# Performance work log

Hardware: AMD Instinct MI355X
Metric: run time of the kernel (lower is better)

## Reference

```python
import jax, jax.numpy as jnp
import numpy as np

EPS = 1e-8  # torch CosineSimilarity default eps


def setup_inputs() -> dict:
    key = jax.random.key(0)
    ks = jax.random.split(key, 9)
    B, C, H, W = 8, 256, 96, 96
    co = C // 2
    s = 0.05
    return {
        "x": jax.random.normal(ks[0], (B, C, H, W), dtype=jnp.float32),
        "w_theta": jax.random.normal(ks[1], (co, C), dtype=jnp.float32) * s,
        "b_theta": jax.random.normal(ks[2], (co,), dtype=jnp.float32) * s,
        "w_phi": jax.random.normal(ks[3], (co, C), dtype=jnp.float32) * s,
        "b_phi": jax.random.normal(ks[4], (co,), dtype=jnp.float32) * s,
        "w_g": jax.random.normal(ks[5], (co, C), dtype=jnp.float32) * s,
        "b_g": jax.random.normal(ks[6], (co,), dtype=jnp.float32) * s,
        "w_back": jax.random.normal(ks[7], (C, co), dtype=jnp.float32) * s,
        "b_back": jax.random.normal(ks[8], (C,), dtype=jnp.float32) * s,
    }


def reference(x, w_theta, b_theta, w_phi, b_phi, w_g, b_g, w_back, b_back):
    B, C, H, W = x.shape
    # replicate pad, then gather the 9 (3x3) shifted views: [B, C, 9, H, W]
    xp = jnp.pad(x, ((0, 0), (0, 0), (1, 1), (1, 1)), mode="edge")
    neigh = jnp.stack(
        [xp[:, :, i:i + H, j:j + W] for i in range(3) for j in range(3)], axis=2
    )
    # 1x1 convs are per-pixel linear maps
    theta = jnp.einsum("bchw,oc->bohw", x, w_theta) + b_theta[None, :, None, None]
    phi = jnp.einsum("bcnhw,oc->bonhw", neigh, w_phi) + b_phi[None, :, None, None, None]
    g = jnp.einsum("bcnhw,oc->bonhw", neigh, w_g) + b_g[None, :, None, None, None]
    # cosine similarity over channel dim o: [B, 9, H, W]
    dot = jnp.sum(phi * theta[:, :, None], axis=1)
    denom = jnp.maximum(
        jnp.sqrt(jnp.sum(phi * phi, axis=1)) * jnp.sqrt(jnp.sum(theta * theta, axis=1))[:, None],
        EPS,
    )
    attn = jax.nn.softmax(dot / denom, axis=1)  # softmax over 9 neighbors
    # weighted average of g over neighbors: [B, co, H, W]
    wa = jnp.einsum("bonhw,bnhw->bohw", g, attn)
    x_res = jnp.einsum("bohw,co->bchw", wa, w_back) + b_back[None, :, None, None]
    return x + x_res
```

## Files before the change

### kernel.cpp

```cpp
#include <hip/hip_runtime.h>
#include <hip/hip_bf16.h>
#include <math.h>

#define HW   9216
#define WIMG 96
#define NPIX 73728
#define CIN  256
#define CO   128

typedef __attribute__((ext_vector_type(8))) short short8v;
typedef __attribute__((ext_vector_type(8))) unsigned short u16x8;
typedef __attribute__((ext_vector_type(4))) float f32x4;

__device__ __forceinline__ unsigned short f2bf(float f) {
    __hip_bfloat16 h = __float2bfloat16(f);
    return __builtin_bit_cast(unsigned short, h);
}
__device__ __forceinline__ float bf2f(unsigned short u) {
    unsigned v = ((unsigned)u) << 16;
    return __builtin_bit_cast(float, v);
}

__device__ __forceinline__ int swz(int row, int kk2 ) {
    return (row * 128 + kk2) ^ ((row & 7) << 4);
}

__global__ __launch_bounds__(256) void k1_mfma(
    const float* __restrict__ x,
    const float* __restrict__ wt, const float* __restrict__ bt,
    const float* __restrict__ wp, const float* __restrict__ bp,
    const float* __restrict__ wg, const float* __restrict__ bg,
    unsigned short* __restrict__ th, unsigned short* __restrict__ ph,
    unsigned short* __restrict__ gf)
{
    __shared__ char As[128 * 128];
    __shared__ char Bs[128 * 128];

    const int t   = threadIdx.x;
    const int bid = blockIdx.x;
    const int lb  = (bid & 7) * 216 + (bid >> 3);
    const int nb  = lb % 3;
    const int bx  = lb / 3;

    const float* W  = (nb == 0) ? wt : (nb == 1) ? wp : wg;
    const float* Bv = (nb == 0) ? bt : (nb == 1) ? bp : bg;
    unsigned short* O = (nb == 0) ? th : (nb == 1) ? ph : gf;

    const int P0 = bx * 128;
    const int b  = P0 / HW;
    const int p0 = P0 - b * HW;
    const float* xb = x + (size_t)b * CIN * HW + p0;

    const int wid = t >> 6, lane = t & 63;
    const int wm = (wid & 1) * 64, wn = (wid >> 1) * 64;
    const int l15 = lane & 15, lg = lane >> 4;

    f32x4 acc[4][4] = {};

    for (int kt = 0; kt < CIN; kt += 64) {
        if (kt) __syncthreads();
        #pragma unroll
        for (int it = 0; it < 8; ++it) {
            int kq = ((t >> 4) & 3) + (it & 3) * 4;
            int pp = (t & 15) + ((t >> 6) << 4) + ((it >> 2) << 6);
            ushort4 v;
            v.x = f2bf(xb[(size_t)(kt + kq * 4 + 0) * HW + pp]);
            v.y = f2bf(xb[(size_t)(kt + kq * 4 + 1) * HW + pp]);
            v.z = f2bf(xb[(size_t)(kt + kq * 4 + 2) * HW + pp]);
            v.w = f2bf(xb[(size_t)(kt + kq * 4 + 3) * HW + pp]);
            *(ushort4*)(As + swz(pp, kq * 8)) = v;
        }
        #pragma unroll
        for (int it = 0; it < 8; ++it) {
            int kq = t & 15;
            int n  = (t >> 4) + it * 16;
            float4 w4 = *(const float4*)(W + (size_t)n * CIN + kt + kq * 4);
            ushort4 v;
            v.x = f2bf(w4.x); v.y = f2bf(w4.y); v.z = f2bf(w4.z); v.w = f2bf(w4.w);
            *(ushort4*)(Bs + swz(n, kq * 8)) = v;
        }
        __syncthreads();
        #pragma unroll
        for (int ks = 0; ks < 2; ++ks) {
            const int kk2 = ks * 64 + lg * 16;
            short8v a[4], bq[4];
            #pragma unroll
            for (int mt = 0; mt < 4; ++mt)
                a[mt] = *(const short8v*)(As + swz(wm + mt * 16 + l15, kk2));
            #pragma unroll
            for (int nt = 0; nt < 4; ++nt)
                bq[nt] = *(const short8v*)(Bs + swz(wn + nt * 16 + l15, kk2));
            #pragma unroll
            for (int mt = 0; mt < 4; ++mt)
                #pragma unroll
                for (int nt = 0; nt < 4; ++nt)
                    acc[mt][nt] = __builtin_amdgcn_mfma_f32_16x16x32_bf16(
                        a[mt], bq[nt], acc[mt][nt], 0, 0, 0);
        }
    }

    float bias[4];
    #pragma unroll
    for (int nt = 0; nt < 4; ++nt) bias[nt] = Bv[wn + nt * 16 + l15];
    #pragma unroll
    for (int mt = 0; mt < 4; ++mt)
        #pragma unroll
        for (int j = 0; j < 4; ++j) {
            size_t row = (size_t)(P0 + wm + mt * 16 + lg * 4 + j) * CO;
            #pragma unroll
            for (int nt = 0; nt < 4; ++nt)
                O[row + wn + nt * 16 + l15] = f2bf(acc[mt][nt][j] + bias[nt]);
        }
}

__global__ __launch_bounds__(256) void k_attn(
    const unsigned short* __restrict__ th, const unsigned short* __restrict__ ph,
    const unsigned short* __restrict__ gf, unsigned short* __restrict__ wa)
{
    const int t   = threadIdx.x;
    const int bid = blockIdx.x;
    const int lb  = (bid & 7) * 144 + (bid >> 3);
    const int s = t >> 2, q = t & 3;
    const int P = lb * 64 + s;
    const int b = P / HW;
    const int p = P - b * HW;
    const int h = p / WIMG;
    const int w = p - h * WIMG;
    const size_t ib = (size_t)b * HW;

    const u16x8* tv = (const u16x8*)(th + (size_t)P * CO + q * 32);
    float T32[32];
    #pragma unroll
    for (int j = 0; j < 4; ++j) {
        u16x8 v = tv[j];
        #pragma unroll
        for (int e = 0; e < 8; ++e) T32[j * 8 + e] = bf2f(v[e]);
    }
    float tt = 0.f;
    #pragma unroll
    for (int k = 0; k < 32; ++k) tt = fmaf(T32[k], T32[k], tt);
    tt += __shfl_xor(tt, 1);
    tt += __shfl_xor(tt, 2);
    const float st = sqrtf(tt);

    float score[9];
    #pragma unroll
    for (int n = 0; n < 9; ++n) {
        int hh = h + n / 3 - 1; hh = hh < 0 ? 0 : (hh > 95 ? 95 : hh);
        int w2 = w + n % 3 - 1; w2 = w2 < 0 ? 0 : (w2 > 95 ? 95 : w2);
        const u16x8* pv = (const u16x8*)(ph + (ib + hh * WIMG + w2) * CO + q * 32);
        float d = 0.f, pp = 0.f;
        #pragma unroll
        for (int j = 0; j < 4; ++j) {
            u16x8 v = pv[j];
            #pragma unroll
            for (int e = 0; e < 8; ++e) {
                float f = bf2f(v[e]);
                d  = fmaf(T32[j * 8 + e], f, d);
                pp = fmaf(f, f, pp);
            }
        }
        d  += __shfl_xor(d, 1);  d  += __shfl_xor(d, 2);
        pp += __shfl_xor(pp, 1); pp += __shfl_xor(pp, 2);
        float den = fmaxf(sqrtf(pp) * st, 1e-8f);
        score[n] = d / den;
    }

    float mx = score[0];
    #pragma unroll
    for (int n = 1; n < 9; ++n) mx = fmaxf(mx, score[n]);
    float sum = 0.f;
    #pragma unroll
    for (int n = 0; n < 9; ++n) { score[n] = expf(score[n] - mx); sum += score[n]; }
    const float inv = 1.f / sum;

    float acc[32];
    #pragma unroll
    for (int k = 0; k < 32; ++k) acc[k] = 0.f;

    #pragma unroll
    for (int n = 0; n < 9; ++n) {
        int hh = h + n / 3 - 1; hh = hh < 0 ? 0 : (hh > 95 ? 95 : hh);
        int w2 = w + n % 3 - 1; w2 = w2 < 0 ? 0 : (w2 > 95 ? 95 : w2);
        const u16x8* gv = (const u16x8*)(gf + (ib + hh * WIMG + w2) * CO + q * 32);
        float a = score[n] * inv;
        #pragma unroll
        for (int j = 0; j < 4; ++j) {
            u16x8 v = gv[j];
            #pragma unroll
            for (int e = 0; e < 8; ++e)
                acc[j * 8 + e] = fmaf(a, bf2f(v[e]), acc[j * 8 + e]);
        }
    }

    u16x8* ov = (u16x8*)(wa + (size_t)P * CO + q * 32);
    #pragma unroll
    for (int j = 0; j < 4; ++j) {
        u16x8 o;
        #pragma unroll
        for (int e = 0; e < 8; ++e) o[e] = f2bf(acc[j * 8 + e]);
        ov[j] = o;
    }
}

__global__ __launch_bounds__(256) void k3_mfma(
    const unsigned short* __restrict__ wa, const float* __restrict__ wb,
    const float* __restrict__ bb_, const float* __restrict__ x,
    float* __restrict__ out)
{
    __shared__ char As[128 * 128];
    __shared__ char Bs[128 * 128];

    const int t   = threadIdx.x;
    const int bid = blockIdx.x;
    const int lb  = (bid & 7) * 144 + (bid >> 3);
    const int cb  = (lb & 1) * 128;
    const int P0  = (lb >> 1) * 128;
    const int b   = P0 / HW;
    const int p0  = P0 - b * HW;

    const int wid = t >> 6, lane = t & 63;
    const int wm = (wid & 1) * 64, wn = (wid >> 1) * 64;
    const int l15 = lane & 15, lg = lane >> 4;

    f32x4 acc[4][4] = {};

    for (int kt = 0; kt < CO; kt += 64) {
        if (kt) __syncthreads();
        #pragma unroll
        for (int it = 0; it < 8; ++it) {
            int kq = t & 15;
            int n  = (t >> 4) + it * 16;
            float4 w4 = *(const float4*)(wb + (size_t)(cb + n) * CO + kt + kq * 4);
            ushort4 v;
            v.x = f2bf(w4.x); v.y = f2bf(w4.y); v.z = f2bf(w4.z); v.w = f2bf(w4.w);
            *(ushort4*)(As + swz(n, kq * 4 * 2)) = v;
        }
        #pragma unroll
        for (int it = 0; it < 4; ++it) {
            int kq = t & 7;
            int n  = (t >> 3) + it * 32;
            u16x8 u = *(const u16x8*)(wa + (size_t)(P0 + n) * CO + kt + kq * 8);
            *(u16x8*)(Bs + swz(n, kq * 16)) = u;
        }
        __syncthreads();
        #pragma unroll
        for (int ks = 0; ks < 2; ++ks) {
            const int kk2 = ks * 64 + lg * 16;
            short8v a[4], bq[4];
            #pragma unroll
            for (int mt = 0; mt < 4; ++mt)
                a[mt] = *(const short8v*)(As + swz(wm + mt * 16 + l15, kk2));
            #pragma unroll
            for (int nt = 0; nt < 4; ++nt)
                bq[nt] = *(const short8v*)(Bs + swz(wn + nt * 16 + l15, kk2));
            #pragma unroll
            for (int mt = 0; mt < 4; ++mt)
                #pragma unroll
                for (int nt = 0; nt < 4; ++nt)
                    acc[mt][nt] = __builtin_amdgcn_mfma_f32_16x16x32_bf16(
                        a[mt], bq[nt], acc[mt][nt], 0, 0, 0);
        }
    }

    #pragma unroll
    for (int mt = 0; mt < 4; ++mt)
        #pragma unroll
        for (int j = 0; j < 4; ++j) {
            int ch = cb + wm + mt * 16 + lg * 4 + j;
            size_t base = ((size_t)b * CIN + ch) * HW + p0;
            float bias = bb_[ch];
            #pragma unroll
            for (int nt = 0; nt < 4; ++nt) {
                int px = wn + nt * 16 + l15;
                out[base + px] = x[base + px] + acc[mt][nt][j] + bias;
            }
        }
}

extern "C" void kernel_launch(void* const* d_in, const int* in_sizes, int n_in,
                              void* d_out, int out_size, void* d_ws, size_t ws_size,
                              hipStream_t stream)
{
    const float* x  = (const float*)d_in[0];
    const float* wt = (const float*)d_in[1];
    const float* bt = (const float*)d_in[2];
    const float* wp = (const float*)d_in[3];
    const float* bp = (const float*)d_in[4];
    const float* wg = (const float*)d_in[5];
    const float* bg = (const float*)d_in[6];
    const float* wb = (const float*)d_in[7];
    const float* bb = (const float*)d_in[8];
    float* out = (float*)d_out;

    const size_t FEAT = (size_t)NPIX * CO;
    unsigned short* th = (unsigned short*)d_ws;
    unsigned short* ph = th + FEAT;
    unsigned short* gf = ph + FEAT;
    unsigned short* wa = gf + FEAT;

    hipLaunchKernelGGL(k1_mfma, dim3(1728), dim3(256), 0, stream,
                       x, wt, bt, wp, bp, wg, bg, th, ph, gf);
    hipLaunchKernelGGL(k_attn, dim3(1152), dim3(256), 0, stream,
                       th, ph, gf, wa);
    hipLaunchKernelGGL(k3_mfma, dim3(1152), dim3(256), 0, stream,
                       wa, wb, bb, x, out);
}
```

Before: 234.4 us.

## Load x tile once per block and reuse it across theta/phi/g projections

The first GEMM kernel now stages the full 128-pixel by 256-channel x tile in LDS as bf16 (64KB) and loops over the three projection weight sets inside one block. Previously each projection launched its own block that re-read and re-converted x. The grid shrinks from 1728 to 576 blocks, which cuts global x traffic threefold but raises LDS use and lowers occupancy and parallelism. The attention kernel also precomputes neighbor offsets, splits the dot-product reductions into four partial accumulators, and uses the fast __expf.

Result: slower. 256.3 us (+9.3%).

```diff
diff --git a/kernel.cpp b/kernel.cpp
--- a/kernel.cpp
+++ b/kernel.cpp
@@ -21,8 +21,11 @@
     return __builtin_bit_cast(float, v);
 }
 
-__device__ __forceinline__ int swz(int row, int kk2 ) {
-    return (row * 128 + kk2) ^ ((row & 7) << 4);
+__device__ __forceinline__ int swz(int row, int kb) {
+    return (row * 128) + (kb ^ ((row & 7) << 4));
+}
+__device__ __forceinline__ int swzA(int row, int kb) {
+    return (row * 512) + (kb ^ ((row & 7) << 4));
 }
 
 __global__ __launch_bounds__(256) void k1_mfma(
@@ -33,32 +36,22 @@
     unsigned short* __restrict__ th, unsigned short* __restrict__ ph,
     unsigned short* __restrict__ gf)
 {
-    __shared__ char As[128 * 128];
+    __shared__ char As[128 * 512];
     __shared__ char Bs[128 * 128];
 
     const int t   = threadIdx.x;
     const int bid = blockIdx.x;
-    const int lb  = (bid & 7) * 216 + (bid >> 3);
-    const int nb  = lb % 3;
-    const int bx  = lb / 3;
-
-    const float* W  = (nb == 0) ? wt : (nb == 1) ? wp : wg;
-    const float* Bv = (nb == 0) ? bt : (nb == 1) ? bp : bg;
-    unsigned short* O = (nb == 0) ? th : (nb == 1) ? ph : gf;
-
-    const int P0 = bx * 128;
-    const int b  = P0 / HW;
-    const int p0 = P0 - b * HW;
+    const int lb  = (bid & 7) * 72 + (bid >> 3);
+    const int P0  = lb * 128;
+    const int b   = P0 / HW;
+    const int p0  = P0 - b * HW;
     const float* xb = x + (size_t)b * CIN * HW + p0;
 
     const int wid = t >> 6, lane = t & 63;
     const int wm = (wid & 1) * 64, wn = (wid >> 1) * 64;
     const int l15 = lane & 15, lg = lane >> 4;
 
-    f32x4 acc[4][4] = {};
-
     for (int kt = 0; kt < CIN; kt += 64) {
-        if (kt) __syncthreads();
         #pragma unroll
         for (int it = 0; it < 8; ++it) {
             int kq = ((t >> 4) & 3) + (it & 3) * 4;
@@ -68,49 +61,62 @@
             v.y = f2bf(xb[(size_t)(kt + kq * 4 + 1) * HW + pp]);
             v.z = f2bf(xb[(size_t)(kt + kq * 4 + 2) * HW + pp]);
             v.w = f2bf(xb[(size_t)(kt + kq * 4 + 3) * HW + pp]);
-            *(ushort4*)(As + swz(pp, kq * 8)) = v;
-        }
-        #pragma unroll
-        for (int it = 0; it < 8; ++it) {
-            int kq = t & 15;
-            int n  = (t >> 4) + it * 16;
-            float4 w4 = *(const float4*)(W + (size_t)n * CIN + kt + kq * 4);
-            ushort4 v;
-            v.x = f2bf(w4.x); v.y = f2bf(w4.y); v.z = f2bf(w4.z); v.w = f2bf(w4.w);
-            *(ushort4*)(Bs + swz(n, kq * 8)) = v;
-        }
-        __syncthreads();
-        #pragma unroll
-        for (int ks = 0; ks < 2; ++ks) {
-            const int kk2 = ks * 64 + lg * 16;
-            short8v a[4], bq[4];
-            #pragma unroll
-            for (int mt = 0; mt < 4; ++mt)
-                a[mt] = *(const short8v*)(As + swz(wm + mt * 16 + l15, kk2));
-            #pragma unroll
-            for (int nt = 0; nt < 4; ++nt)
-                bq[nt] = *(const short8v*)(Bs + swz(wn + nt * 16 + l15, kk2));
-            #pragma unroll
-            for (int mt = 0; mt < 4; ++mt)
+            *(ushort4*)(As + swzA(pp, (kt + kq * 4) * 2)) = v;
+        }
+    }
+
+    for (int nb = 0; nb < 3; ++nb) {
+        const float* W  = (nb == 0) ? wt : (nb == 1) ? wp : wg;
+        const float* Bv = (nb == 0) ? bt : (nb == 1) ? bp : bg;
+        unsigned short* O = (nb == 0) ? th : (nb == 1) ? ph : gf;
+
+        f32x4 acc[4][4] = {};
+
+        for (int kt = 0; kt < CIN; kt += 64) {
+            __syncthreads();
+            #pragma unroll
+            for (int it = 0; it < 8; ++it) {
+                int kq = t & 15;
+                int n  = (t >> 4) + it * 16;
+                float4 w4 = *(const float4*)(W + (size_t)n * CIN + kt + kq * 4);
+                ushort4 v;
+                v.x = f2bf(w4.x); v.y = f2bf(w4.y); v.z = f2bf(w4.z); v.w = f2bf(w4.w);
+                *(ushort4*)(Bs + swz(n, kq * 8)) = v;
+            }
+            __syncthreads();
+            #pragma unroll
+            for (int ks = 0; ks < 2; ++ks) {
+                const int akb = kt * 2 + ks * 64 + lg * 16;
+                const int bkb = ks * 64 + lg * 16;
+                short8v a[4], bq[4];
+                #pragma unroll
+                for (int mt = 0; mt < 4; ++mt)
+                    a[mt] = *(const short8v*)(As + swzA(wm + mt * 16 + l15, akb));
                 #pragma unroll
                 for (int nt = 0; nt < 4; ++nt)
-                    acc[mt][nt] = __builtin_amdgcn_mfma_f32_16x16x32_bf16(
-                        a[mt], bq[nt], acc[mt][nt], 0, 0, 0);
-        }
-    }
-
-    float bias[4];
-    #pragma unroll
-    for (int nt = 0; nt < 4; ++nt) bias[nt] = Bv[wn + nt * 16 + l15];
-    #pragma unroll
-    for (int mt = 0; mt < 4; ++mt)
-        #pragma unroll
-        for (int j = 0; j < 4; ++j) {
-            size_t row = (size_t)(P0 + wm + mt * 16 + lg * 4 + j) * CO;
-            #pragma unroll
-            for (int nt = 0; nt < 4; ++nt)
-                O[row + wn + nt * 16 + l15] = f2bf(acc[mt][nt][j] + bias[nt]);
-        }
+                    bq[nt] = *(const short8v*)(Bs + swz(wn + nt * 16 + l15, bkb));
+                #pragma unroll
+                for (int mt = 0; mt < 4; ++mt)
+                    #pragma unroll
+                    for (int nt = 0; nt < 4; ++nt)
+                        acc[mt][nt] = __builtin_amdgcn_mfma_f32_16x16x32_bf16(
+                            a[mt], bq[nt], acc[mt][nt], 0, 0, 0);
+            }
+        }
+
+        float bias[4];
+        #pragma unroll
+        for (int nt = 0; nt < 4; ++nt) bias[nt] = Bv[wn + nt * 16 + l15];
+        #pragma unroll
+        for (int mt = 0; mt < 4; ++mt)
+            #pragma unroll
+            for (int j = 0; j < 4; ++j) {
+                size_t row = (size_t)(P0 + wm + mt * 16 + lg * 4 + j) * CO;
+                #pragma unroll
+                for (int nt = 0; nt < 4; ++nt)
+                    O[row + wn + nt * 16 + l15] = f2bf(acc[mt][nt][j] + bias[nt]);
+            }
+    }
 }
 
 __global__ __launch_bounds__(256) void k_attn(
@@ -128,6 +134,14 @@
     const int w = p - h * WIMG;
     const size_t ib = (size_t)b * HW;
 
+    size_t nbase[9];
+    #pragma unroll
+    for (int n = 0; n < 9; ++n) {
+        int hh = h + n / 3 - 1; hh = hh < 0 ? 0 : (hh > 95 ? 95 : hh);
+        int w2 = w + n % 3 - 1; w2 = w2 < 0 ? 0 : (w2 > 95 ? 95 : w2);
+        nbase[n] = (ib + (size_t)hh * WIMG + w2) * CO + q * 32;
+    }
+
     const u16x8* tv = (const u16x8*)(th + (size_t)P * CO + q * 32);
     float T32[32];
     #pragma unroll
@@ -136,9 +150,13 @@
         #pragma unroll
         for (int e = 0; e < 8; ++e) T32[j * 8 + e] = bf2f(v[e]);
     }
-    float tt = 0.f;
-    #pragma unroll
-    for (int k = 0; k < 32; ++k) tt = fmaf(T32[k], T32[k], tt);
+    float t4[4] = {0.f, 0.f, 0.f, 0.f};
+    #pragma unroll
+    for (int j = 0; j < 4; ++j)
+        #pragma unroll
+        for (int e = 0; e < 8; ++e)
+            t4[j] = fmaf(T32[j * 8 + e], T32[j * 8 + e], t4[j]);
+    float tt = (t4[0] + t4[1]) + (t4[2] + t4[3]);
     tt += __shfl_xor(tt, 1);
     tt += __shfl_xor(tt, 2);
     const float st = sqrtf(tt);
@@ -146,20 +164,21 @@
     float score[9];
     #pragma unroll
     for (int n = 0; n < 9; ++n) {
-        int hh = h + n / 3 - 1; hh = hh < 0 ? 0 : (hh > 95 ? 95 : hh);
-        int w2 = w + n % 3 - 1; w2 = w2 < 0 ? 0 : (w2 > 95 ? 95 : w2);
-        const u16x8* pv = (const u16x8*)(ph + (ib + hh * WIMG + w2) * CO + q * 32);
-        float d = 0.f, pp = 0.f;
+        const u16x8* pv = (const u16x8*)(ph + nbase[n]);
+        float d4[4] = {0.f, 0.f, 0.f, 0.f};
+        float p4[4] = {0.f, 0.f, 0.f, 0.f};
         #pragma unroll
         for (int j = 0; j < 4; ++j) {
             u16x8 v = pv[j];
             #pragma unroll
             for (int e = 0; e < 8; ++e) {
                 float f = bf2f(v[e]);
-                d  = fmaf(T32[j * 8 + e], f, d);
-                pp = fmaf(f, f, pp);
-            }
-        }
+                d4[j] = fmaf(T32[j * 8 + e], f, d4[j]);
+                p4[j] = fmaf(f, f, p4[j]);
+            }
+        }
+        float d  = (d4[0] + d4[1]) + (d4[2] + d4[3]);
+        float pp = (p4[0] + p4[1]) + (p4[2] + p4[3]);
         d  += __shfl_xor(d, 1);  d  += __shfl_xor(d, 2);
         pp += __shfl_xor(pp, 1); pp += __shfl_xor(pp, 2);
         float den = fmaxf(sqrtf(pp) * st, 1e-8f);
@@ -171,7 +190,7 @@
     for (int n = 1; n < 9; ++n) mx = fmaxf(mx, score[n]);
     float sum = 0.f;
     #pragma unroll
-    for (int n = 0; n < 9; ++n) { score[n] = expf(score[n] - mx); sum += score[n]; }
+    for (int n = 0; n < 9; ++n) { score[n] = __expf(score[n] - mx); sum += score[n]; }
     const float inv = 1.f / sum;
 
     float acc[32];
@@ -180,9 +199,7 @@
 
     #pragma unroll
     for (int n = 0; n < 9; ++n) {
-        int hh = h + n / 3 - 1; hh = hh < 0 ? 0 : (hh > 95 ? 95 : hh);
-        int w2 = w + n % 3 - 1; w2 = w2 < 0 ? 0 : (w2 > 95 ? 95 : w2);
-        const u16x8* gv = (const u16x8*)(gf + (ib + hh * WIMG + w2) * CO + q * 32);
+        const u16x8* gv = (const u16x8*)(gf + nbase[n]);
         float a = score[n] * inv;
         #pragma unroll
         for (int j = 0; j < 4; ++j) {
@@ -234,7 +251,7 @@
             float4 w4 = *(const float4*)(wb + (size_t)(cb + n) * CO + kt + kq * 4);
             ushort4 v;
             v.x = f2bf(w4.x); v.y = f2bf(w4.y); v.z = f2bf(w4.z); v.w = f2bf(w4.w);
-            *(ushort4*)(As + swz(n, kq * 4 * 2)) = v;
+            *(ushort4*)(As + swz(n, kq * 8)) = v;
         }
         #pragma unroll
         for (int it = 0; it < 4; ++it) {
@@ -299,7 +316,7 @@
     unsigned short* gf = ph + FEAT;
     unsigned short* wa = gf + FEAT;
 
-    hipLaunchKernelGGL(k1_mfma, dim3(1728), dim3(256), 0, stream,
+    hipLaunchKernelGGL(k1_mfma, dim3(576), dim3(256), 0, stream,
                        x, wt, bt, wp, bp, wg, bg, th, ph, gf);
     hipLaunchKernelGGL(k_attn, dim3(1152), dim3(256), 0, stream,
                        th, ph, gf, wa);
```
